# Kernel optimization log

Hardware: AMD Instinct MI355X
Metric: run time of the kernel (lower is better)

Reference implementation:

```python
import jax, jax.numpy as jnp
import numpy as np

NQ = 10000   # num_q
N = 512      # n (seq len)
D = 512      # d (model dim)
H = 8        # attention heads
LW = 64      # local window
B = 16       # batch


def _mha(q, k, v, wi, bi, wo, bo, nh, mask=None):
    # torch nn.MultiheadAttention math (eval mode, dropout off), batch-first inputs
    Bq, S, d = q.shape
    hd = d // nh
    wq, wk, wv = jnp.split(wi, 3, axis=0)
    bq, bk, bv = jnp.split(bi, 3)

    def proj(x, w, b):
        y = x @ w.T + b
        return y.reshape(x.shape[0], x.shape[1], nh, hd).transpose(0, 2, 1, 3)  # [B,h,S,hd]

    Q = proj(q, wq, bq)
    K = proj(k, wk, bk)
    V = proj(v, wv, bv)
    s = jnp.einsum('bhqe,bhke->bhqk', Q, K) / jnp.sqrt(jnp.asarray(hd, q.dtype))
    if mask is not None:
        s = jnp.where(mask[None, None], -jnp.inf, s)
    w = jax.nn.softmax(s, axis=-1)
    o = jnp.einsum('bhqk,bhke->bhqe', w, V).transpose(0, 2, 1, 3).reshape(Bq, S, d)
    return o @ wo.T + bo, w.mean(axis=1)  # avg over heads like torch default


def _ln(x, g, b):
    m = x.mean(-1, keepdims=True)
    v = ((x - m) ** 2).mean(-1, keepdims=True)
    return (x - m) / jnp.sqrt(v + 1e-5) * g + b


def setup_inputs() -> dict:
    key = jax.random.key(0)
    ks = iter(jax.random.split(key, 40))
    f = lambda *sh: jax.random.normal(next(ks), sh, jnp.float32) * 0.02
    inp = {
        'q': jax.random.randint(next(ks), (B, N), 0, NQ, jnp.int32),
        'r': jax.random.randint(next(ks), (B, N), 0, 2, jnp.int32),
        'qry': jax.random.randint(next(ks), (B, N), 0, NQ, jnp.int32),
        'M_emb': f(2 * NQ, D),
        'E_emb': f(NQ, D),
        'P': f(N, D),
    }
    for nm in ['base', 'local', 'glob', 'cross']:
        inp[nm + '_in_w'] = f(3 * D, D)
        inp[nm + '_in_b'] = jnp.zeros((3 * D,), jnp.float32)
        inp[nm + '_out_w'] = f(D, D)
        inp[nm + '_out_b'] = jnp.zeros((D,), jnp.float32)
    inp['ln1_g'] = jnp.ones((D,), jnp.float32)
    inp['ln1_b'] = jnp.zeros((D,), jnp.float32)
    inp['w1'] = f(D, D)
    inp['b1'] = jnp.zeros((D,), jnp.float32)
    inp['w2'] = f(D, D)
    inp['b2'] = jnp.zeros((D,), jnp.float32)
    inp['ln2_g'] = jnp.ones((D,), jnp.float32)
    inp['ln2_b'] = jnp.zeros((D,), jnp.float32)
    inp['pred_w'] = f(1, D)
    inp['pred_b'] = jnp.zeros((1,), jnp.float32)
    return inp


def reference(q, r, qry, M_emb, E_emb, P,
              base_in_w, base_in_b, base_out_w, base_out_b,
              local_in_w, local_in_b, local_out_w, local_out_b,
              glob_in_w, glob_in_b, glob_out_w, glob_out_b,
              cross_in_w, cross_in_b, cross_out_w, cross_out_b,
              ln1_g, ln1_b, w1, b1, w2, b2, ln2_g, ln2_b, pred_w, pred_b):
    x = q + NQ * r
    M = M_emb[x] + P[None]          # [B,N,D], positional added as in torch code
    E = E_emb[qry]                  # [B,N,D]
    cm = jnp.triu(jnp.ones((N, N), bool), 1)

    S_base, attn_w = _mha(E, M, M, base_in_w, base_in_b, base_out_w, base_out_b, H, cm)
    S_base = _ln(S_base + M + E, ln1_g, ln1_b)

    lm = jnp.triu(jnp.ones((LW, LW), bool), 1)
    s_loc_in = S_base[:, -LW:, :]
    S_loc, _ = _mha(s_loc_in, s_loc_in, s_loc_in, local_in_w, local_in_b, local_out_w, local_out_b, H, lm)
    S_local = jnp.concatenate([jnp.zeros((S_base.shape[0], N - LW, D), S_base.dtype), S_loc], axis=1)

    S_global, _ = _mha(S_base, S_base, S_base, glob_in_w, glob_in_b, glob_out_w, glob_out_b, H, cm)
    S_cross, _ = _mha(S_base, S_local, S_local, cross_in_w, cross_in_b, cross_out_w, cross_out_b, H, None)

    S = S_base + S_local + S_global + S_cross
    F = jax.nn.relu(S @ w1.T + b1) @ w2.T + b2
    F = _ln(F + S, ln2_g, ln2_b)
    p = jax.nn.sigmoid(F @ pred_w.T + pred_b)[..., 0]   # [B,N]
    return p, attn_w
```

## Files before the change

### kernel.cpp

```cpp
#include <hip/hip_runtime.h>
#include <hip/hip_bf16.h>

#define D_MODEL 512
#define NHEAD 8
#define NSEQ 512
#define BATCH 16
#define LWIN 64
#define S2C 0.18033688f
#define L2E 1.44269504f

typedef short s16x8 __attribute__((ext_vector_type(8)));
typedef float f32x4 __attribute__((ext_vector_type(4)));

__device__ inline unsigned short f2bf(float f) {
    unsigned int u = __float_as_uint(f);
    u = (u + 0x7fffu + ((u >> 16) & 1u)) >> 16;
    return (unsigned short)u;
}

struct WP { const float* p[10]; };
__global__ __launch_bounds__(256) void wconv_kernel(WP wp, unsigned short* __restrict__ Wb)
{
    const long e = ((long)blockIdx.x * 256 + threadIdx.x) * 4;
    const float* src; long loc;
    if (e < 3145728) { int rg = (int)(e / 786432); src = wp.p[rg]; loc = e - (long)rg * 786432; }
    else { long j = e - 3145728; int rg = (int)(j >> 18); src = wp.p[4 + rg]; loc = j - ((long)rg << 18); }
    float4 v = *(const float4*)(src + loc);
    ushort4 o; o.x = f2bf(v.x); o.y = f2bf(v.y); o.z = f2bf(v.z); o.w = f2bf(v.w);
    *(ushort4*)(Wb + e) = o;
}

__global__ __launch_bounds__(128) void embed_kernel(
    const int* __restrict__ q, const int* __restrict__ r, const int* __restrict__ qry,
    const float* __restrict__ M_emb, const float* __restrict__ E_emb,
    const float* __restrict__ P, float* __restrict__ Mf, float* __restrict__ Ef,
    unsigned short* __restrict__ Mb, unsigned short* __restrict__ Eb)
{
    const int t = blockIdx.x;
    const int n = t & (NSEQ - 1);
    const int x = q[t] + 10000 * r[t];
    const int e = qry[t];
    const int i = threadIdx.x;
    float4 a = ((const float4*)(M_emb + (long)x * D_MODEL))[i];
    float4 p4 = ((const float4*)(P + (long)n * D_MODEL))[i];
    float4 ev = ((const float4*)(E_emb + (long)e * D_MODEL))[i];
    float4 mv = make_float4(a.x + p4.x, a.y + p4.y, a.z + p4.z, a.w + p4.w);
    ((float4*)(Mf + (long)t * D_MODEL))[i] = mv;
    ((float4*)(Ef + (long)t * D_MODEL))[i] = ev;
    ushort4 mb; mb.x = f2bf(mv.x); mb.y = f2bf(mv.y); mb.z = f2bf(mv.z); mb.w = f2bf(mv.w);
    ushort4 eb; eb.x = f2bf(ev.x); eb.y = f2bf(ev.y); eb.z = f2bf(ev.z); eb.w = f2bf(ev.w);
    *(ushort4*)(Mb + (long)t * D_MODEL + i * 4) = mb;
    *(ushort4*)(Eb + (long)t * D_MODEL + i * 4) = eb;
}

__global__ __launch_bounds__(256) void gemm_bf16(
    const unsigned short* __restrict__ A, const unsigned short* __restrict__ A2, int nsplit,
    const unsigned short* __restrict__ W, const float* __restrict__ bias,
    unsigned short* __restrict__ Cb, float* __restrict__ Cf, int ldc, int relu, int arem)
{
    __shared__ unsigned short As[128 * 40];
    __shared__ unsigned short Ws[128 * 40];
    const int tid = threadIdx.x, lane = tid & 63, wid = tid >> 6;
    const int m0 = blockIdx.y * 128, n0 = blockIdx.x * 128;
    const int mbase = (wid >> 1) * 64, nbase = (wid & 1) * 64;
    const int srow = tid >> 2, scol = (tid & 3) * 8;
    const unsigned short* Asel = (n0 >= nsplit) ? A2 : A;
    int row0 = m0 + srow, row1 = m0 + srow + 64;
    if (arem) {
        row0 = ((row0 >> 6) << 9) + (NSEQ - LWIN) + (row0 & 63);
        row1 = ((row1 >> 6) << 9) + (NSEQ - LWIN) + (row1 & 63);
    }
    const unsigned short* Ap0 = Asel + (long)row0 * 512 + scol;
    const unsigned short* Ap1 = Asel + (long)row1 * 512 + scol;
    const unsigned short* Wp = W + (long)(n0 + srow) * 512 + scol;
    const int fr = lane & 15;
    const int fk = (lane >> 4) * 8;

    f32x4 acc[4][4];
    #pragma unroll
    for (int i = 0; i < 4; ++i)
        #pragma unroll
        for (int j = 0; j < 4; ++j) acc[i][j] = (f32x4){0.f, 0.f, 0.f, 0.f};

    for (int k0 = 0; k0 < 512; k0 += 32) {
        s16x8 a0 = *(const s16x8*)(Ap0 + k0);
        s16x8 a1 = *(const s16x8*)(Ap1 + k0);
        s16x8 w0 = *(const s16x8*)(Wp + k0);
        s16x8 w1 = *(const s16x8*)(Wp + 64 * 512 + k0);
        __syncthreads();
        *(s16x8*)&As[srow * 40 + scol] = a0;
        *(s16x8*)&As[(64 + srow) * 40 + scol] = a1;
        *(s16x8*)&Ws[srow * 40 + scol] = w0;
        *(s16x8*)&Ws[(64 + srow) * 40 + scol] = w1;
        __syncthreads();
        s16x8 af[4], wf[4];
        #pragma unroll
        for (int t = 0; t < 4; ++t) {
            af[t] = *(const s16x8*)&As[(mbase + t * 16 + fr) * 40 + fk];
            wf[t] = *(const s16x8*)&Ws[(nbase + t * 16 + fr) * 40 + fk];
        }
        #pragma unroll
        for (int i = 0; i < 4; ++i)
            #pragma unroll
            for (int j = 0; j < 4; ++j)
                acc[i][j] = __builtin_amdgcn_mfma_f32_16x16x32_bf16(af[i], wf[j], acc[i][j], 0, 0, 0);
    }

    const int q4 = (lane >> 4) * 4;
    #pragma unroll
    for (int j = 0; j < 4; ++j) {
        const int col = n0 + nbase + j * 16 + fr;
        const float bv = bias[col];
        #pragma unroll
        for (int i = 0; i < 4; ++i) {
            const int row = m0 + mbase + i * 16 + q4;
            #pragma unroll
            for (int rg = 0; rg < 4; ++rg) {
                float v = acc[i][j][rg] + bv;
                if (relu) v = fmaxf(v, 0.f);
                const long off = (long)(row + rg) * ldc + col;
                if (Cb) Cb[off] = f2bf(v);
                if (Cf) Cf[off] = v;
            }
        }
    }
}

__global__ __launch_bounds__(256) void flash_mfma(
    const unsigned short* __restrict__ Q, const unsigned short* __restrict__ K,
    const unsigned short* __restrict__ V, unsigned short* __restrict__ O,
    float* __restrict__ stats, int Nq, int Nkv, int ldq, int ldkv, int causal)
{
    __shared__ __align__(16) unsigned short Ks[64 * 72];
    __shared__ __align__(16) unsigned short Pl[64 * 72];
    __shared__ __align__(16) unsigned int   Vt[64 * 36];

    const int tid = threadIdx.x, lane = tid & 63, w = tid >> 6;
    const int lm = lane & 15, lq = lane >> 4;
    const int h = blockIdx.y, b = blockIdx.z;
    const int nqt = Nq >> 6;
    const int qa = blockIdx.x, qb = nqt - 1 - qa;
    const bool single = (qa == qb);

    s16x8 aqA0, aqA1, aqB0, aqB1;
    {
        const unsigned short* qp = Q + ((long)b * Nq + qb * 64 + w * 16 + lm) * ldq + h * 64 + lq * 8;
        aqB0 = *(const s16x8*)qp; aqB1 = *(const s16x8*)(qp + 32);
    }
    if (!single) {
        const unsigned short* qp = Q + ((long)b * Nq + qa * 64 + w * 16 + lm) * ldq + h * 64 + lq * 8;
        aqA0 = *(const s16x8*)qp; aqA1 = *(const s16x8*)(qp + 32);
    }

    float mA = -INFINITY, lA = 0.f, mB = -INFINITY, lB = 0.f;
    f32x4 oA[4], oB[4];
    #pragma unroll
    for (int t = 0; t < 4; ++t) { oA[t] = (f32x4){0.f,0.f,0.f,0.f}; oB[t] = (f32x4){0.f,0.f,0.f,0.f}; }

    const int nkt = causal ? (qb + 1) : (Nkv >> 6);
    const int skey = tid >> 3, sd = (tid & 7) * 8;

    s16x8 kr0, kr1; uint4 vr0, vr1;
    {
        const long kb = ((long)b * Nkv) * ldkv + h * 64;
        kr0 = *(const s16x8*)(K + kb + (long)skey * ldkv + sd);
        kr1 = *(const s16x8*)(K + kb + (long)(skey + 32) * ldkv + sd);
        const unsigned short* vp = V + ((long)b * Nkv + 2 * skey) * ldkv + h * 64 + sd;
        vr0 = *(const uint4*)vp; vr1 = *(const uint4*)(vp + ldkv);
    }

    auto process = [&](s16x8 a0, s16x8 a1, float& m, float& l, f32x4* oacc, bool diag) {
        f32x4 sc[4];
        #pragma unroll
        for (int t = 0; t < 4; ++t) sc[t] = (f32x4){0.f,0.f,0.f,0.f};
        #pragma unroll
        for (int t = 0; t < 4; ++t) {
            s16x8 k0 = *(const s16x8*)&Ks[(t * 16 + lm) * 72 + lq * 8];
            s16x8 k1 = *(const s16x8*)&Ks[(t * 16 + lm) * 72 + lq * 8 + 32];
            sc[t] = __builtin_amdgcn_mfma_f32_16x16x32_bf16(k0, a0, sc[t], 0, 0, 0);
            sc[t] = __builtin_amdgcn_mfma_f32_16x16x32_bf16(k1, a1, sc[t], 0, 0, 0);
        }
        if (diag) {
            #pragma unroll
            for (int t = 0; t < 4; ++t)
                #pragma unroll
                for (int r = 0; r < 4; ++r)
                    if (t * 16 + lq * 4 + r > w * 16 + lm) sc[t][r] = -INFINITY;
        }
        float mt = sc[0][0];
        #pragma unroll
        for (int t = 0; t < 4; ++t)
            #pragma unroll
            for (int r = 0; r < 4; ++r) mt = fmaxf(mt, sc[t][r]);
        mt = fmaxf(mt, __shfl_xor(mt, 16));
        mt = fmaxf(mt, __shfl_xor(mt, 32));
        const float mn = fmaxf(m, mt);
        const float al = exp2f((m - mn) * S2C);
        float rs = 0.f;
        #pragma unroll
        for (int t = 0; t < 4; ++t)
            #pragma unroll
            for (int r = 0; r < 4; ++r) {
                float p = exp2f((sc[t][r] - mn) * S2C);
                sc[t][r] = p; rs += p;
            }
        rs += __shfl_xor(rs, 16);
        rs += __shfl_xor(rs, 32);
        m = mn; l = l * al + rs;
        #pragma unroll
        for (int t = 0; t < 4; ++t) oacc[t] *= al;
        #pragma unroll
        for (int t = 0; t < 4; ++t) {
            ushort4 u;
            u.x = f2bf(sc[t][0]); u.y = f2bf(sc[t][1]);
            u.z = f2bf(sc[t][2]); u.w = f2bf(sc[t][3]);
            *(ushort4*)&Pl[(w * 16 + lm) * 72 + t * 16 + lq * 4] = u;
        }
        #pragma unroll
        for (int ks = 0; ks < 2; ++ks) {
            s16x8 bp = *(const s16x8*)&Pl[(w * 16 + lm) * 72 + ks * 32 + lq * 8];
            #pragma unroll
            for (int t = 0; t < 4; ++t) {
                const int row = t * 16 + lm;
                const int pg = ((lq >> 1) + 2 * ks) ^ ((row >> 3) & 3);
                s16x8 av = *(const s16x8*)((const unsigned short*)Vt + row * 72 + pg * 16 + (lq & 1) * 8);
                oacc[t] = __builtin_amdgcn_mfma_f32_16x16x32_bf16(av, bp, oacc[t], 0, 0, 0);
            }
        }
    };

    for (int kt = 0; kt < nkt; ++kt) {
        __syncthreads();
        *(s16x8*)&Ks[skey * 72 + sd] = kr0;
        *(s16x8*)&Ks[(skey + 32) * 72 + sd] = kr1;
        {
            unsigned pw[8];
            pw[0] = (vr0.x & 0xffffu) | (vr1.x << 16);
            pw[1] = (vr0.x >> 16)     | (vr1.x & 0xffff0000u);
            pw[2] = (vr0.y & 0xffffu) | (vr1.y << 16);
            pw[3] = (vr0.y >> 16)     | (vr1.y & 0xffff0000u);
            pw[4] = (vr0.z & 0xffffu) | (vr1.z << 16);
            pw[5] = (vr0.z >> 16)     | (vr1.z & 0xffff0000u);
            pw[6] = (vr0.w & 0xffffu) | (vr1.w << 16);
            pw[7] = (vr0.w >> 16)     | (vr1.w & 0xffff0000u);
            #pragma unroll
            for (int j = 0; j < 8; ++j) {
                const int row = sd + j;
                const int col = (((skey >> 3) ^ ((row >> 3) & 3)) << 3) | (skey & 7);
                Vt[row * 36 + col] = pw[j];
            }
        }
        __syncthreads();
        if (kt + 1 < nkt) {
            const long kb = ((long)b * Nkv + (kt + 1) * 64) * ldkv + h * 64;
            kr0 = *(const s16x8*)(K + kb + (long)skey * ldkv + sd);
            kr1 = *(const s16x8*)(K + kb + (long)(skey + 32) * ldkv + sd);
            const unsigned short* vp = V + ((long)b * Nkv + (kt + 1) * 64 + 2 * skey) * ldkv + h * 64 + sd;
            vr0 = *(const uint4*)vp; vr1 = *(const uint4*)(vp + ldkv);
        }
        process(aqB0, aqB1, mB, lB, oB, causal && (kt == qb));
        if (!single && (!causal || kt <= qa))
            process(aqA0, aqA1, mA, lA, oA, causal && (kt == qa));
    }

    {
        const float inv = 1.0f / lB;
        const long orow = ((long)b * Nq + qb * 64 + w * 16 + lm) * D_MODEL + h * 64;
        #pragma unroll
        for (int t = 0; t < 4; ++t) {
            ushort4 u;
            u.x = f2bf(oB[t][0] * inv); u.y = f2bf(oB[t][1] * inv);
            u.z = f2bf(oB[t][2] * inv); u.w = f2bf(oB[t][3] * inv);
            *(ushort4*)(O + orow + t * 16 + lq * 4) = u;
        }
    }
    if (!single) {
        const float inv = 1.0f / lA;
        const long orow = ((long)b * Nq + qa * 64 + w * 16 + lm) * D_MODEL + h * 64;
        #pragma unroll
        for (int t = 0; t < 4; ++t) {
            ushort4 u;
            u.x = f2bf(oA[t][0] * inv); u.y = f2bf(oA[t][1] * inv);
            u.z = f2bf(oA[t][2] * inv); u.w = f2bf(oA[t][3] * inv);
            *(ushort4*)(O + orow + t * 16 + lq * 4) = u;
        }
    }
    if (stats && lq == 0) {
        long idx = (((long)b * NHEAD + h) * Nq + qb * 64 + w * 16 + lm) * 2;
        stats[idx] = mB * 0.125f; stats[idx + 1] = lB;
        if (!single) {
            idx = (((long)b * NHEAD + h) * Nq + qa * 64 + w * 16 + lm) * 2;
            stats[idx] = mA * 0.125f; stats[idx + 1] = lA;
        }
    }
}

__global__ __launch_bounds__(256) void attn_w_kernel(
    const unsigned short* __restrict__ Q, const unsigned short* __restrict__ K,
    const float* __restrict__ stats, float* __restrict__ AW, int ldq, int ldk)
{
    const int kt = blockIdx.x, qt = blockIdx.y, b = blockIdx.z;
    const int tid = threadIdx.x;
    if (kt > qt) {
        const int tx = tid & 15, ty = tid >> 4;
        #pragma unroll
        for (int i = 0; i < 4; ++i)
            *(float4*)(AW + ((long)b * NSEQ + qt * 64 + ty * 4 + i) * NSEQ + kt * 64 + tx * 4)
                = make_float4(0.f, 0.f, 0.f, 0.f);
        return;
    }
    __shared__ __align__(16) unsigned short Ks[64 * 72];
    const int lane = tid & 63, w = tid >> 6;
    const int lm = lane & 15, lq = lane >> 4;
    const int skey = tid >> 3, sd = (tid & 7) * 8;
    const long qrow = (long)b * NSEQ + qt * 64 + w * 16 + lm;

    f32x4 aw[4];
    #pragma unroll
    for (int t = 0; t < 4; ++t) aw[t] = (f32x4){0.f,0.f,0.f,0.f};

    for (int h = 0; h < NHEAD; ++h) {
        __syncthreads();
        {
            const long kb = ((long)b * NSEQ + kt * 64) * ldk + h * 64;
            *(s16x8*)&Ks[skey * 72 + sd] = *(const s16x8*)(K + kb + (long)skey * ldk + sd);
            *(s16x8*)&Ks[(skey + 32) * 72 + sd] = *(const s16x8*)(K + kb + (long)(skey + 32) * ldk + sd);
        }
        __syncthreads();
        s16x8 a0, a1;
        {
            const unsigned short* qp = Q + qrow * ldq + h * 64 + lq * 8;
            a0 = *(const s16x8*)qp; a1 = *(const s16x8*)(qp + 32);
        }
        f32x4 sc[4];
        #pragma unroll
        for (int t = 0; t < 4; ++t) sc[t] = (f32x4){0.f,0.f,0.f,0.f};
        #pragma unroll
        for (int t = 0; t < 4; ++t) {
            s16x8 k0 = *(const s16x8*)&Ks[(t * 16 + lm) * 72 + lq * 8];
            s16x8 k1 = *(const s16x8*)&Ks[(t * 16 + lm) * 72 + lq * 8 + 32];
            sc[t] = __builtin_amdgcn_mfma_f32_16x16x32_bf16(k0, a0, sc[t], 0, 0, 0);
            sc[t] = __builtin_amdgcn_mfma_f32_16x16x32_bf16(k1, a1, sc[t], 0, 0, 0);
        }
        float2 ml = *(const float2*)(stats + (((long)b * NHEAD + h) * NSEQ + qt * 64 + w * 16 + lm) * 2);
        const float mb2 = ml.x * L2E;
        const float sca = 0.125f / ml.y;
        #pragma unroll
        for (int t = 0; t < 4; ++t)
            #pragma unroll
            for (int r = 0; r < 4; ++r) {
                const bool masked = (kt == qt) && (t * 16 + lq * 4 + r > w * 16 + lm);
                if (!masked) aw[t][r] += exp2f(sc[t][r] * S2C - mb2) * sca;
            }
    }
    #pragma unroll
    for (int t = 0; t < 4; ++t)
        *(float4*)(AW + qrow * NSEQ + kt * 64 + t * 16 + lq * 4) = float4{aw[t][0], aw[t][1], aw[t][2], aw[t][3]};
}

__global__ __launch_bounds__(256) void ln_kernel(
    const float* __restrict__ X, const float* __restrict__ R1,
    const float* __restrict__ R2, const float* __restrict__ g,
    const float* __restrict__ bb, float* __restrict__ outf,
    unsigned short* __restrict__ outb)
{
    const long row = blockIdx.x;
    const int tid = threadIdx.x;
    __shared__ float red[256];
    const long base = row * D_MODEL;
    float v0 = X[base + tid], v1 = X[base + tid + 256];
    if (R1) { v0 += R1[base + tid]; v1 += R1[base + tid + 256]; }
    if (R2) { v0 += R2[base + tid]; v1 += R2[base + tid + 256]; }
    red[tid] = v0 + v1; __syncthreads();
    for (int s = 128; s > 0; s >>= 1) {
        if (tid < s) red[tid] += red[tid + s];
        __syncthreads();
    }
    const float mean = red[0] * (1.f / 512.f);
    __syncthreads();
    const float d0 = v0 - mean, d1 = v1 - mean;
    red[tid] = d0 * d0 + d1 * d1; __syncthreads();
    for (int s = 128; s > 0; s >>= 1) {
        if (tid < s) red[tid] += red[tid + s];
        __syncthreads();
    }
    const float rstd = rsqrtf(red[0] * (1.f / 512.f) + 1e-5f);
    const float y0 = d0 * rstd * g[tid] + bb[tid];
    const float y1 = d1 * rstd * g[tid + 256] + bb[tid + 256];
    if (outf) { outf[base + tid] = y0; outf[base + tid + 256] = y1; }
    if (outb) { outb[base + tid] = f2bf(y0); outb[base + tid + 256] = f2bf(y1); }
}

__global__ __launch_bounds__(128) void build_slocal(
    const float* __restrict__ Tloc, float* __restrict__ Sf, unsigned short* __restrict__ Sb)
{
    const int t = blockIdx.x;
    const int b = t >> 9, n = t & 511;
    const int i = threadIdx.x;
    float4 v;
    if (n < NSEQ - LWIN) v = make_float4(0.f, 0.f, 0.f, 0.f);
    else v = ((const float4*)(Tloc + ((long)b * LWIN + (n - (NSEQ - LWIN))) * D_MODEL))[i];
    ((float4*)(Sf + (long)t * D_MODEL))[i] = v;
    ushort4 u; u.x = f2bf(v.x); u.y = f2bf(v.y); u.z = f2bf(v.z); u.w = f2bf(v.w);
    *(ushort4*)(Sb + (long)t * D_MODEL + i * 4) = u;
}

__global__ __launch_bounds__(256) void sum4_kernel(
    const float* __restrict__ a, const float* __restrict__ b,
    const float* __restrict__ c, const float* __restrict__ d,
    float* __restrict__ of, unsigned short* __restrict__ ob, int n4)
{
    const int i = blockIdx.x * blockDim.x + threadIdx.x;
    if (i < n4) {
        float4 x = ((const float4*)a)[i];
        float4 y = ((const float4*)b)[i];
        float4 z = ((const float4*)c)[i];
        float4 w = ((const float4*)d)[i];
        float4 s = make_float4(x.x + y.x + z.x + w.x, x.y + y.y + z.y + w.y,
                               x.z + y.z + z.z + w.z, x.w + y.w + z.w + w.w);
        ((float4*)of)[i] = s;
        ushort4 u; u.x = f2bf(s.x); u.y = f2bf(s.y); u.z = f2bf(s.z); u.w = f2bf(s.w);
        *(ushort4*)(ob + (long)i * 4) = u;
    }
}

__global__ __launch_bounds__(256) void pred_kernel(
    const float* __restrict__ F, const float* __restrict__ pw,
    const float* __restrict__ pb, float* __restrict__ out)
{
    const int w = threadIdx.x >> 6, lane = threadIdx.x & 63;
    const long row = (long)blockIdx.x * 4 + w;
    const float* fr = F + row * D_MODEL;
    float s = 0.f;
    #pragma unroll
    for (int i = 0; i < 8; ++i) s += fr[lane + i * 64] * pw[lane + i * 64];
    #pragma unroll
    for (int off = 32; off > 0; off >>= 1) s += __shfl_down(s, off);
    if (lane == 0) out[row] = 1.f / (1.f + __expf(-(s + pb[0])));
}

extern "C" void kernel_launch(void* const* d_in, const int* in_sizes, int n_in,
                              void* d_out, int out_size, void* d_ws, size_t ws_size,
                              hipStream_t stream)
{
    const int*   q          = (const int*)d_in[0];
    const int*   r          = (const int*)d_in[1];
    const int*   qry        = (const int*)d_in[2];
    const float* M_emb      = (const float*)d_in[3];
    const float* E_emb      = (const float*)d_in[4];
    const float* P          = (const float*)d_in[5];
    const float* base_in_w  = (const float*)d_in[6];
    const float* base_in_b  = (const float*)d_in[7];
    const float* base_out_w = (const float*)d_in[8];
    const float* base_out_b = (const float*)d_in[9];
    const float* local_in_w = (const float*)d_in[10];
    const float* local_in_b = (const float*)d_in[11];
    const float* local_out_w= (const float*)d_in[12];
    const float* local_out_b= (const float*)d_in[13];
    const float* glob_in_w  = (const float*)d_in[14];
    const float* glob_in_b  = (const float*)d_in[15];
    const float* glob_out_w = (const float*)d_in[16];
    const float* glob_out_b = (const float*)d_in[17];
    const float* cross_in_w = (const float*)d_in[18];
    const float* cross_in_b = (const float*)d_in[19];
    const float* cross_out_w= (const float*)d_in[20];
    const float* cross_out_b= (const float*)d_in[21];
    const float* ln1_g      = (const float*)d_in[22];
    const float* ln1_b      = (const float*)d_in[23];
    const float* w1         = (const float*)d_in[24];
    const float* b1         = (const float*)d_in[25];
    const float* w2         = (const float*)d_in[26];
    const float* b2         = (const float*)d_in[27];
    const float* ln2_g      = (const float*)d_in[28];
    const float* ln2_b      = (const float*)d_in[29];
    const float* pred_w     = (const float*)d_in[30];
    const float* pred_b     = (const float*)d_in[31];
    float* out = (float*)d_out;

    char* p = (char*)d_ws;
    unsigned short* Wb = (unsigned short*)p; p += 4718592L * 2;
    unsigned short* B[11];
    for (int i = 0; i < 11; ++i) { B[i] = (unsigned short*)p; p += 8388608L; }
    unsigned short* Obl  = (unsigned short*)p; p += 1048576L;
    float* R[5];
    for (int i = 0; i < 5; ++i) { R[i] = (float*)p; p += 16777216L; }
    float* Tloc  = (float*)p; p += 2097152L;
    float* stats = (float*)p; p += 524288L;

    unsigned short* Mb = B[0];
    unsigned short* Eb = B[1];      unsigned short* Oc_b = B[1];
    unsigned short* QKVb = B[2];
    unsigned short* Sb_b = B[2];
    unsigned short* Ob  = B[5];
    unsigned short* Sbase_b  = B[6];
    unsigned short* Slocal_b = B[7];
    unsigned short* QKV3 = B[8];
    unsigned short* H1_b = B[8];
    float* Mf = R[0];       float* Scross_f = R[0];
    float* Ef = R[1];       float* Sbuf_f   = R[1];
    float* Tb_f = R[2];     float* Sglobal_f= R[2];  float* Fbuf_f = R[2];
    float* Sbase_f = R[3];  float* Fpre_f   = R[3];
    float* Slocal_f = R[4];

    const long oBin = 0, oLin = 786432, oGin = 1572864, oCin = 2359296;
    const long oBout = 3145728, oLout = 3407872, oGout = 3670016, oCout = 3932160;
    const long oW1 = 4194304, oW2 = 4456448;
    const int BIG = 1 << 30;

    dim3 gN512(4, 64), gN1536(12, 64);
    dim3 gL1536(12, 8), gL512(4, 8);
    dim3 fa_full(4, NHEAD, BATCH), fa_loc(1, NHEAD, BATCH);

    WP wp; wp.p[0] = base_in_w; wp.p[1] = local_in_w; wp.p[2] = glob_in_w; wp.p[3] = cross_in_w;
    wp.p[4] = base_out_w; wp.p[5] = local_out_w; wp.p[6] = glob_out_w; wp.p[7] = cross_out_w;
    wp.p[8] = w1; wp.p[9] = w2;
    wconv_kernel<<<4608, 256, 0, stream>>>(wp, Wb);

    embed_kernel<<<8192, 128, 0, stream>>>(q, r, qry, M_emb, E_emb, P, Mf, Ef, Mb, Eb);

    gemm_bf16<<<gN1536, 256, 0, stream>>>(Eb, Mb, 512, Wb + oBin, base_in_b, QKVb, nullptr, 1536, 0, 0);
    flash_mfma<<<fa_full, 256, 0, stream>>>(QKVb, QKVb + 512, QKVb + 1024, Ob, stats, 512, 512, 1536, 1536, 1);
    attn_w_kernel<<<dim3(8, 8, BATCH), 256, 0, stream>>>(QKVb, QKVb + 512, stats, out + 8192, 1536, 1536);
    gemm_bf16<<<gN512, 256, 0, stream>>>(Ob, Ob, BIG, Wb + oBout, base_out_b, nullptr, Tb_f, 512, 0, 0);
    ln_kernel<<<8192, 256, 0, stream>>>(Tb_f, Mf, Ef, ln1_g, ln1_b, Sbase_f, Sbase_b);

    gemm_bf16<<<gL1536, 256, 0, stream>>>(Sbase_b, Sbase_b, BIG, Wb + oLin, local_in_b, QKV3, nullptr, 1536, 0, 1);
    flash_mfma<<<fa_loc, 256, 0, stream>>>(QKV3, QKV3 + 512, QKV3 + 1024, Obl, nullptr, 64, 64, 1536, 1536, 1);
    gemm_bf16<<<gL512, 256, 0, stream>>>(Obl, Obl, BIG, Wb + oLout, local_out_b, nullptr, Tloc, 512, 0, 0);
    build_slocal<<<8192, 128, 0, stream>>>(Tloc, Slocal_f, Slocal_b);

    gemm_bf16<<<gN1536, 256, 0, stream>>>(Sbase_b, Sbase_b, BIG, Wb + oGin, glob_in_b, QKV3, nullptr, 1536, 0, 0);
    flash_mfma<<<fa_full, 256, 0, stream>>>(QKV3, QKV3 + 512, QKV3 + 1024, Ob, nullptr, 512, 512, 1536, 1536, 1);
    gemm_bf16<<<gN512, 256, 0, stream>>>(Ob, Ob, BIG, Wb + oGout, glob_out_b, nullptr, Sglobal_f, 512, 0, 0);

    gemm_bf16<<<gN1536, 256, 0, stream>>>(Sbase_b, Slocal_b, 512, Wb + oCin, cross_in_b, QKVb, nullptr, 1536, 0, 0);
    flash_mfma<<<fa_full, 256, 0, stream>>>(QKVb, QKVb + 512, QKVb + 1024, Oc_b, nullptr, 512, 512, 1536, 1536, 0);
    gemm_bf16<<<gN512, 256, 0, stream>>>(Oc_b, Oc_b, BIG, Wb + oCout, cross_out_b, nullptr, Scross_f, 512, 0, 0);

    const int n4 = (int)((long)BATCH * NSEQ * D_MODEL / 4);
    sum4_kernel<<<(n4 + 255) / 256, 256, 0, stream>>>(Sbase_f, Slocal_f, Sglobal_f, Scross_f, Sbuf_f, Sb_b, n4);

    gemm_bf16<<<gN512, 256, 0, stream>>>(Sb_b, Sb_b, BIG, Wb + oW1, b1, H1_b, nullptr, 512, 1, 0);
    gemm_bf16<<<gN512, 256, 0, stream>>>(H1_b, H1_b, BIG, Wb + oW2, b2, nullptr, Fpre_f, 512, 0, 0);
    ln_kernel<<<8192, 256, 0, stream>>>(Fpre_f, Sbuf_f, nullptr, ln2_g, ln2_b, Fbuf_f, nullptr);
    pred_kernel<<<2048, 256, 0, stream>>>(Fbuf_f, pred_w, pred_b, out);
}
```

Measured before the change: 534.8 us.

## Fuse residual sum and pred into GEMM/LN epilogues, use direct-to-LDS swizzled loads

```diff
diff --git a/kernel.cpp b/kernel.cpp
--- a/kernel.cpp
+++ b/kernel.cpp
@@ -17,6 +17,11 @@
     u = (u + 0x7fffu + ((u >> 16) & 1u)) >> 16;
     return (unsigned short)u;
 }
+__device__ inline int sw4(int r) { return (r + (r >> 2)) & 3; }
+
+#define GLD16(g, l) __builtin_amdgcn_global_load_lds( \
+    (const __attribute__((address_space(1))) void*)(g), \
+    (__attribute__((address_space(3))) void*)(l), 16, 0, 0)
 
 struct WP { const float* p[10]; };
 __global__ __launch_bounds__(256) void wconv_kernel(WP wp, unsigned short* __restrict__ Wb)
@@ -53,28 +58,47 @@
     *(ushort4*)(Eb + (long)t * D_MODEL + i * 4) = eb;
 }
 
+__global__ __launch_bounds__(256) void zfill_kernel(unsigned short* __restrict__ p)
+{
+    const long i = ((long)blockIdx.x * 256 + threadIdx.x) * 8;
+    *(uint4*)(p + i) = make_uint4(0u, 0u, 0u, 0u);
+}
+
 __global__ __launch_bounds__(256) void gemm_bf16(
     const unsigned short* __restrict__ A, const unsigned short* __restrict__ A2, int nsplit,
     const unsigned short* __restrict__ W, const float* __restrict__ bias,
-    unsigned short* __restrict__ Cb, float* __restrict__ Cf, int ldc, int relu, int arem)
-{
-    __shared__ unsigned short As[128 * 40];
-    __shared__ unsigned short Ws[128 * 40];
+    unsigned short* __restrict__ Cb, int ldcb, int crem,
+    float* __restrict__ Cf, int ldcf,
+    const float* __restrict__ r1, const float* __restrict__ r2, const float* __restrict__ tl,
+    int relu, int arem)
+{
+    __shared__ __align__(16) unsigned short Sh[8704];
+    unsigned short* As = Sh;
+    unsigned short* Ws = Sh + 4096;
+    float* Shf = (float*)Sh;
+
     const int tid = threadIdx.x, lane = tid & 63, wid = tid >> 6;
     const int m0 = blockIdx.y * 128, n0 = blockIdx.x * 128;
     const int mbase = (wid >> 1) * 64, nbase = (wid & 1) * 64;
-    const int srow = tid >> 2, scol = (tid & 3) * 8;
+    const int fr = lane & 15;
+    const int lq = lane >> 4;
     const unsigned short* Asel = (n0 >= nsplit) ? A2 : A;
-    int row0 = m0 + srow, row1 = m0 + srow + 64;
+
+    const int rlane = lane >> 2, clane = lane & 3;
+    const int lrA0 = wid * 16 + rlane, lrA1 = 64 + wid * 16 + rlane;
+    int rgA0 = m0 + lrA0, rgA1 = m0 + lrA1;
     if (arem) {
-        row0 = ((row0 >> 6) << 9) + (NSEQ - LWIN) + (row0 & 63);
-        row1 = ((row1 >> 6) << 9) + (NSEQ - LWIN) + (row1 & 63);
-    }
-    const unsigned short* Ap0 = Asel + (long)row0 * 512 + scol;
-    const unsigned short* Ap1 = Asel + (long)row1 * 512 + scol;
-    const unsigned short* Wp = W + (long)(n0 + srow) * 512 + scol;
-    const int fr = lane & 15;
-    const int fk = (lane >> 4) * 8;
+        rgA0 = ((rgA0 >> 6) << 9) + (NSEQ - LWIN) + (rgA0 & 63);
+        rgA1 = ((rgA1 >> 6) << 9) + (NSEQ - LWIN) + (rgA1 & 63);
+    }
+    const unsigned short* pA0 = Asel + (long)rgA0 * 512 + ((clane ^ sw4(lrA0)) << 3);
+    const unsigned short* pA1 = Asel + (long)rgA1 * 512 + ((clane ^ sw4(lrA1)) << 3);
+    const unsigned short* pW0 = W + (long)(n0 + lrA0) * 512 + ((clane ^ sw4(lrA0)) << 3);
+    const unsigned short* pW1 = W + (long)(n0 + lrA1) * 512 + ((clane ^ sw4(lrA1)) << 3);
+    unsigned short* lA0 = As + (wid * 16) * 32;
+    unsigned short* lA1 = As + (64 + wid * 16) * 32;
+    unsigned short* lW0 = Ws + (wid * 16) * 32;
+    unsigned short* lW1 = Ws + (64 + wid * 16) * 32;
 
     f32x4 acc[4][4];
     #pragma unroll
@@ -83,21 +107,20 @@
         for (int j = 0; j < 4; ++j) acc[i][j] = (f32x4){0.f, 0.f, 0.f, 0.f};
 
     for (int k0 = 0; k0 < 512; k0 += 32) {
-        s16x8 a0 = *(const s16x8*)(Ap0 + k0);
-        s16x8 a1 = *(const s16x8*)(Ap1 + k0);
-        s16x8 w0 = *(const s16x8*)(Wp + k0);
-        s16x8 w1 = *(const s16x8*)(Wp + 64 * 512 + k0);
-        __syncthreads();
-        *(s16x8*)&As[srow * 40 + scol] = a0;
-        *(s16x8*)&As[(64 + srow) * 40 + scol] = a1;
-        *(s16x8*)&Ws[srow * 40 + scol] = w0;
-        *(s16x8*)&Ws[(64 + srow) * 40 + scol] = w1;
-        __syncthreads();
+        __syncthreads();
+        GLD16(pA0 + k0, lA0);
+        GLD16(pA1 + k0, lA1);
+        GLD16(pW0 + k0, lW0);
+        GLD16(pW1 + k0, lW1);
+        __syncthreads();
+
         s16x8 af[4], wf[4];
         #pragma unroll
         for (int t = 0; t < 4; ++t) {
-            af[t] = *(const s16x8*)&As[(mbase + t * 16 + fr) * 40 + fk];
-            wf[t] = *(const s16x8*)&Ws[(nbase + t * 16 + fr) * 40 + fk];
+            const int ra = mbase + t * 16 + fr;
+            const int rw = nbase + t * 16 + fr;
+            af[t] = *(const s16x8*)&As[ra * 32 + ((lq ^ sw4(ra)) << 3)];
+            wf[t] = *(const s16x8*)&Ws[rw * 32 + ((lq ^ sw4(rw)) << 3)];
         }
         #pragma unroll
         for (int i = 0; i < 4; ++i)
@@ -107,20 +130,49 @@
     }
 
     const int q4 = (lane >> 4) * 4;
-    #pragma unroll
-    for (int j = 0; j < 4; ++j) {
-        const int col = n0 + nbase + j * 16 + fr;
-        const float bv = bias[col];
-        #pragma unroll
-        for (int i = 0; i < 4; ++i) {
-            const int row = m0 + mbase + i * 16 + q4;
-            #pragma unroll
-            for (int rg = 0; rg < 4; ++rg) {
-                float v = acc[i][j][rg] + bv;
-                if (relu) v = fmaxf(v, 0.f);
-                const long off = (long)(row + rg) * ldc + col;
-                if (Cb) Cb[off] = f2bf(v);
-                if (Cf) Cf[off] = v;
+    for (int qtr = 0; qtr < 4; ++qtr) {
+        __syncthreads();
+        if ((wid >> 1) == (qtr >> 1)) {
+            const int ibase = (qtr & 1) * 2;
+            #pragma unroll
+            for (int j = 0; j < 4; ++j) {
+                const int lcol = nbase + j * 16 + fr;
+                const float bv = bias[n0 + lcol];
+                #pragma unroll
+                for (int i2 = 0; i2 < 2; ++i2) {
+                    const int i = ibase + i2;
+                    #pragma unroll
+                    for (int rg = 0; rg < 4; ++rg) {
+                        float v = acc[i][j][rg] + bv;
+                        if (relu) v = fmaxf(v, 0.f);
+                        Shf[((i * 16 + q4 + rg) & 31) * 132 + lcol] = v;
+                    }
+                }
+            }
+        }
+        __syncthreads();
+        #pragma unroll
+        for (int it = 0; it < 4; ++it) {
+            const int flat = it * 256 + tid;
+            const int rowq = flat >> 5, k4 = flat & 31;
+            const int grow = m0 + qtr * 32 + rowq;
+            const int gcol = n0 + k4 * 4;
+            float4 f = *(const float4*)&Shf[rowq * 132 + k4 * 4];
+            if (r1) {
+                float4 a = *(const float4*)(r1 + (long)grow * 512 + gcol);
+                float4 b = *(const float4*)(r2 + (long)grow * 512 + gcol);
+                f.x += a.x + b.x; f.y += a.y + b.y; f.z += a.z + b.z; f.w += a.w + b.w;
+                const int n = grow & 511;
+                if (n >= NSEQ - LWIN) {
+                    float4 c = *(const float4*)(tl + ((long)(grow >> 9) * 64 + (n - (NSEQ - LWIN))) * 512 + gcol);
+                    f.x += c.x; f.y += c.y; f.z += c.z; f.w += c.w;
+                }
+            }
+            if (Cf) *(float4*)(Cf + (long)grow * ldcf + gcol) = f;
+            if (Cb) {
+                const int crow = crem ? (((grow >> 6) << 9) + (NSEQ - LWIN) + (grow & 63)) : grow;
+                ushort4 u; u.x = f2bf(f.x); u.y = f2bf(f.y); u.z = f2bf(f.z); u.w = f2bf(f.w);
+                *(ushort4*)(Cb + (long)crow * ldcb + gcol) = u;
             }
         }
     }
@@ -362,7 +414,9 @@
     const float* __restrict__ X, const float* __restrict__ R1,
     const float* __restrict__ R2, const float* __restrict__ g,
     const float* __restrict__ bb, float* __restrict__ outf,
-    unsigned short* __restrict__ outb)
+    unsigned short* __restrict__ outb,
+    const float* __restrict__ pw, const float* __restrict__ pb,
+    float* __restrict__ outp)
 {
     const long row = blockIdx.x;
     const int tid = threadIdx.x;
@@ -387,56 +441,19 @@
     const float rstd = rsqrtf(red[0] * (1.f / 512.f) + 1e-5f);
     const float y0 = d0 * rstd * g[tid] + bb[tid];
     const float y1 = d1 * rstd * g[tid + 256] + bb[tid + 256];
+    if (pw) {
+        float s = y0 * pw[tid] + y1 * pw[tid + 256];
+        __syncthreads();
+        red[tid] = s; __syncthreads();
+        for (int st = 128; st > 0; st >>= 1) {
+            if (tid < st) red[tid] += red[tid + st];
+            __syncthreads();
+        }
+        if (tid == 0) outp[row] = 1.f / (1.f + __expf(-(red[0] + pb[0])));
+        return;
+    }
     if (outf) { outf[base + tid] = y0; outf[base + tid + 256] = y1; }
     if (outb) { outb[base + tid] = f2bf(y0); outb[base + tid + 256] = f2bf(y1); }
-}
-
-__global__ __launch_bounds__(128) void build_slocal(
-    const float* __restrict__ Tloc, float* __restrict__ Sf, unsigned short* __restrict__ Sb)
-{
-    const int t = blockIdx.x;
-    const int b = t >> 9, n = t & 511;
-    const int i = threadIdx.x;
-    float4 v;
-    if (n < NSEQ - LWIN) v = make_float4(0.f, 0.f, 0.f, 0.f);
-    else v = ((const float4*)(Tloc + ((long)b * LWIN + (n - (NSEQ - LWIN))) * D_MODEL))[i];
-    ((float4*)(Sf + (long)t * D_MODEL))[i] = v;
-    ushort4 u; u.x = f2bf(v.x); u.y = f2bf(v.y); u.z = f2bf(v.z); u.w = f2bf(v.w);
-    *(ushort4*)(Sb + (long)t * D_MODEL + i * 4) = u;
-}
-
-__global__ __launch_bounds__(256) void sum4_kernel(
-    const float* __restrict__ a, const float* __restrict__ b,
-    const float* __restrict__ c, const float* __restrict__ d,
-    float* __restrict__ of, unsigned short* __restrict__ ob, int n4)
-{
-    const int i = blockIdx.x * blockDim.x + threadIdx.x;
-    if (i < n4) {
-        float4 x = ((const float4*)a)[i];
-        float4 y = ((const float4*)b)[i];
-        float4 z = ((const float4*)c)[i];
-        float4 w = ((const float4*)d)[i];
-        float4 s = make_float4(x.x + y.x + z.x + w.x, x.y + y.y + z.y + w.y,
-                               x.z + y.z + z.z + w.z, x.w + y.w + z.w + w.w);
-        ((float4*)of)[i] = s;
-        ushort4 u; u.x = f2bf(s.x); u.y = f2bf(s.y); u.z = f2bf(s.z); u.w = f2bf(s.w);
-        *(ushort4*)(ob + (long)i * 4) = u;
-    }
-}
-
-__global__ __launch_bounds__(256) void pred_kernel(
-    const float* __restrict__ F, const float* __restrict__ pw,
-    const float* __restrict__ pb, float* __restrict__ out)
-{
-    const int w = threadIdx.x >> 6, lane = threadIdx.x & 63;
-    const long row = (long)blockIdx.x * 4 + w;
-    const float* fr = F + row * D_MODEL;
-    float s = 0.f;
-    #pragma unroll
-    for (int i = 0; i < 8; ++i) s += fr[lane + i * 64] * pw[lane + i * 64];
-    #pragma unroll
-    for (int off = 32; off > 0; off >>= 1) s += __shfl_down(s, off);
-    if (lane == 0) out[row] = 1.f / (1.f + __expf(-(s + pb[0])));
 }
 
 extern "C" void kernel_launch(void* const* d_in, const int* in_sizes, int n_in,
@@ -482,8 +499,8 @@
     unsigned short* B[11];
     for (int i = 0; i < 11; ++i) { B[i] = (unsigned short*)p; p += 8388608L; }
     unsigned short* Obl  = (unsigned short*)p; p += 1048576L;
-    float* R[5];
-    for (int i = 0; i < 5; ++i) { R[i] = (float*)p; p += 16777216L; }
+    float* R[4];
+    for (int i = 0; i < 4; ++i) { R[i] = (float*)p; p += 16777216L; }
     float* Tloc  = (float*)p; p += 2097152L;
     float* stats = (float*)p; p += 524288L;
 
@@ -496,16 +513,17 @@
     unsigned short* Slocal_b = B[7];
     unsigned short* QKV3 = B[8];
     unsigned short* H1_b = B[8];
-    float* Mf = R[0];       float* Scross_f = R[0];
+    float* Mf = R[0];
     float* Ef = R[1];       float* Sbuf_f   = R[1];
-    float* Tb_f = R[2];     float* Sglobal_f= R[2];  float* Fbuf_f = R[2];
+    float* Tb_f = R[2];     float* Sglobal_f= R[2];
     float* Sbase_f = R[3];  float* Fpre_f   = R[3];
-    float* Slocal_f = R[4];
 
     const long oBin = 0, oLin = 786432, oGin = 1572864, oCin = 2359296;
     const long oBout = 3145728, oLout = 3407872, oGout = 3670016, oCout = 3932160;
     const long oW1 = 4194304, oW2 = 4456448;
     const int BIG = 1 << 30;
+    const unsigned short* NUS = nullptr;
+    const float* NF = nullptr;
 
     dim3 gN512(4, 64), gN1536(12, 64);
     dim3 gL1536(12, 8), gL512(4, 8);
@@ -515,33 +533,40 @@
     wp.p[4] = base_out_w; wp.p[5] = local_out_w; wp.p[6] = glob_out_w; wp.p[7] = cross_out_w;
     wp.p[8] = w1; wp.p[9] = w2;
     wconv_kernel<<<4608, 256, 0, stream>>>(wp, Wb);
+    zfill_kernel<<<2048, 256, 0, stream>>>(Slocal_b);
 
     embed_kernel<<<8192, 128, 0, stream>>>(q, r, qry, M_emb, E_emb, P, Mf, Ef, Mb, Eb);
 
-    gemm_bf16<<<gN1536, 256, 0, stream>>>(Eb, Mb, 512, Wb + oBin, base_in_b, QKVb, nullptr, 1536, 0, 0);
+    gemm_bf16<<<gN1536, 256, 0, stream>>>(Eb, Mb, 512, Wb + oBin, base_in_b,
+        QKVb, 1536, 0, nullptr, 0, NF, NF, NF, 0, 0);
     flash_mfma<<<fa_full, 256, 0, stream>>>(QKVb, QKVb + 512, QKVb + 1024, Ob, stats, 512, 512, 1536, 1536, 1);
     attn_w_kernel<<<dim3(8, 8, BATCH), 256, 0, stream>>>(QKVb, QKVb + 512, stats, out + 8192, 1536, 1536);
-    gemm_bf16<<<gN512, 256, 0, stream>>>(Ob, Ob, BIG, Wb + oBout, base_out_b, nullptr, Tb_f, 512, 0, 0);
-    ln_kernel<<<8192, 256, 0, stream>>>(Tb_f, Mf, Ef, ln1_g, ln1_b, Sbase_f, Sbase_b);
-
-    gemm_bf16<<<gL1536, 256, 0, stream>>>(Sbase_b, Sbase_b, BIG, Wb + oLin, local_in_b, QKV3, nullptr, 1536, 0, 1);
+    gemm_bf16<<<gN512, 256, 0, stream>>>(Ob, NUS, BIG, Wb + oBout, base_out_b,
+        nullptr, 0, 0, Tb_f, 512, NF, NF, NF, 0, 0);
+    ln_kernel<<<8192, 256, 0, stream>>>(Tb_f, Mf, Ef, ln1_g, ln1_b, Sbase_f, Sbase_b, NF, NF, nullptr);
+
+    gemm_bf16<<<gL1536, 256, 0, stream>>>(Sbase_b, NUS, BIG, Wb + oLin, local_in_b,
+        QKV3, 1536, 0, nullptr, 0, NF, NF, NF, 0, 1);
     flash_mfma<<<fa_loc, 256, 0, stream>>>(QKV3, QKV3 + 512, QKV3 + 1024, Obl, nullptr, 64, 64, 1536, 1536, 1);
-    gemm_bf16<<<gL512, 256, 0, stream>>>(Obl, Obl, BIG, Wb + oLout, local_out_b, nullptr, Tloc, 512, 0, 0);
-    build_slocal<<<8192, 128, 0, stream>>>(Tloc, Slocal_f, Slocal_b);
-
-    gemm_bf16<<<gN1536, 256, 0, stream>>>(Sbase_b, Sbase_b, BIG, Wb + oGin, glob_in_b, QKV3, nullptr, 1536, 0, 0);
+    gemm_bf16<<<gL512, 256, 0, stream>>>(Obl, NUS, BIG, Wb + oLout, local_out_b,
+        Slocal_b, 512, 1, Tloc, 512, NF, NF, NF, 0, 0);
+
+    gemm_bf16<<<gN1536, 256, 0, stream>>>(Sbase_b, NUS, BIG, Wb + oGin, glob_in_b,
+        QKV3, 1536, 0, nullptr, 0, NF, NF, NF, 0, 0);
     flash_mfma<<<fa_full, 256, 0, stream>>>(QKV3, QKV3 + 512, QKV3 + 1024, Ob, nullptr, 512, 512, 1536, 1536, 1);
-    gemm_bf16<<<gN512, 256, 0, stream>>>(Ob, Ob, BIG, Wb + oGout, glob_out_b, nullptr, Sglobal_f, 512, 0, 0);
-
-    gemm_bf16<<<gN1536, 256, 0, stream>>>(Sbase_b, Slocal_b, 512, Wb + oCin, cross_in_b, QKVb, nullptr, 1536, 0, 0);
+    gemm_bf16<<<gN512, 256, 0, stream>>>(Ob, NUS, BIG, Wb + oGout, glob_out_b,
+        nullptr, 0, 0, Sglobal_f, 512, NF, NF, NF, 0, 0);
+
+    gemm_bf16<<<gN1536, 256, 0, stream>>>(Sbase_b, Slocal_b, 512, Wb + oCin, cross_in_b,
+        QKVb, 1536, 0, nullptr, 0, NF, NF, NF, 0, 0);
     flash_mfma<<<fa_full, 256, 0, stream>>>(QKVb, QKVb + 512, QKVb + 1024, Oc_b, nullptr, 512, 512, 1536, 1536, 0);
-    gemm_bf16<<<gN512, 256, 0, stream>>>(Oc_b, Oc_b, BIG, Wb + oCout, cross_out_b, nullptr, Scross_f, 512, 0, 0);
-
-    const int n4 = (int)((long)BATCH * NSEQ * D_MODEL / 4);
-    sum4_kernel<<<(n4 + 255) / 256, 256, 0, stream>>>(Sbase_f, Slocal_f, Sglobal_f, Scross_f, Sbuf_f, Sb_b, n4);
-
-    gemm_bf16<<<gN512, 256, 0, stream>>>(Sb_b, Sb_b, BIG, Wb + oW1, b1, H1_b, nullptr, 512, 1, 0);
-    gemm_bf16<<<gN512, 256, 0, stream>>>(H1_b, H1_b, BIG, Wb + oW2, b2, nullptr, Fpre_f, 512, 0, 0);
-    ln_kernel<<<8192, 256, 0, stream>>>(Fpre_f, Sbuf_f, nullptr, ln2_g, ln2_b, Fbuf_f, nullptr);
-    pred_kernel<<<2048, 256, 0, stream>>>(Fbuf_f, pred_w, pred_b, out);
-}
+    gemm_bf16<<<gN512, 256, 0, stream>>>(Oc_b, NUS, BIG, Wb + oCout, cross_out_b,
+        Sb_b, 512, 0, Sbuf_f, 512, Sbase_f, Sglobal_f, Tloc, 0, 0);
+
+    gemm_bf16<<<gN512, 256, 0, stream>>>(Sb_b, NUS, BIG, Wb + oW1, b1,
+        H1_b, 512, 0, nullptr, 0, NF, NF, NF, 1, 0);
+    gemm_bf16<<<gN512, 256, 0, stream>>>(H1_b, NUS, BIG, Wb + oW2, b2,
+        nullptr, 0, 0, Fpre_f, 512, NF, NF, NF, 0, 0);
+    ln_kernel<<<8192, 256, 0, stream>>>(Fpre_f, Sbuf_f, nullptr, ln2_g, ln2_b,
+        nullptr, nullptr, pred_w, pred_b, out);
+}
```

New measurement: 526.7 us. No clear change (-1.5%).
